# Kernel tuning notes

Measured on AMD Instinct MI355X. Metric: run time of the kernel, lower is better.

Reference implementation:

```python
import jax, jax.numpy as jnp
import numpy as np
import math

N_H = 16
REL_K = 16  # relative-position clamp window


def setup_inputs() -> dict:
    key = jax.random.key(0)
    ks = jax.random.split(key, 7)
    B, S, D = 8, 1024, 1024
    d_k = D // N_H
    scale = 0.02
    return {
        "x": jax.random.normal(ks[0], (B, S, D), dtype=jnp.float32),
        "W_attn": jax.random.normal(ks[1], (D, 3 * D), dtype=jnp.float32) * scale,
        "b_attn": jax.random.normal(ks[2], (3 * D,), dtype=jnp.float32) * scale,
        "W_proj": jax.random.normal(ks[3], (D, D), dtype=jnp.float32) * scale,
        "b_proj": jax.random.normal(ks[4], (D,), dtype=jnp.float32) * scale,
        "lut_k": jax.random.normal(ks[5], (2 * REL_K + 1, d_k), dtype=jnp.float32) * scale,
        "lut_v": jax.random.normal(ks[6], (2 * REL_K + 1, d_k), dtype=jnp.float32) * scale,
    }


def reference(x, W_attn, b_attn, W_proj, b_proj, lut_k, lut_v):
    B, S, D = x.shape
    d_k = D // N_H

    qkv = x @ W_attn + b_attn  # [B, S, 3D]
    q, k, v = jnp.split(qkv, 3, axis=-1)
    # [B, H, S, d_k]
    q = q.reshape(B, S, N_H, d_k).transpose(0, 2, 1, 3)
    k = k.reshape(B, S, N_H, d_k).transpose(0, 2, 1, 3)
    v = v.reshape(B, S, N_H, d_k).transpose(0, 2, 1, 3)

    i = jnp.arange(S)[:, None]
    j = jnp.arange(S)[None, :]
    rel = jnp.clip(j - i, -REL_K, REL_K) + REL_K  # [S, S] in [0, 2k]
    aij_k = lut_k[rel]  # [S, S, d_k]
    aij_v = lut_v[rel]  # [S, S, d_k]

    scores = jnp.einsum('bhid,bhjd->bhij', q, k)
    scores = scores + jnp.einsum('bhid,ijd->bhij', q, aij_k)
    scores = scores * (1.0 / math.sqrt(d_k))

    causal = j <= i  # [S, S]
    scores = jnp.where(causal[None, None, :, :], scores, -jnp.inf)
    attn = jax.nn.softmax(scores, axis=-1)  # [B, H, S, S]

    out = jnp.einsum('bhij,bhjd->bhid', attn, v)
    out = out + jnp.einsum('bhij,ijd->bhid', attn, aij_v)
    out = out.transpose(0, 2, 1, 3).reshape(B, S, D)
    return out @ W_proj + b_proj
```

## Files before the change

kernel.cpp:

```cpp
#include <hip/hip_runtime.h>
#include <hip/hip_bf16.h>
#include <math.h>

#define NH 16
#define S_LEN 1024
#define DK 64
#define D_MODEL 1024
#define HSZ 8388608

typedef __attribute__((ext_vector_type(8))) short bf16x8;
typedef __attribute__((ext_vector_type(4))) float f32x4;
typedef unsigned short USH;

#define EXPSCALE 0.1803368801111204f

__device__ __forceinline__ float fast_exp2(float x) {
    return __builtin_amdgcn_exp2f(x);
}

__device__ __forceinline__ short f2b(float x) {
    union { __hip_bfloat16 h; short s; } u;
    u.h = __float2bfloat16(x);
    return u.s;
}
__device__ __forceinline__ float b2f(USH u) {
    union { unsigned i; float f; } x;
    x.i = (unsigned)u << 16;
    return x.f;
}

__device__ __forceinline__ void gload16(const void* src, void* lds) {
    __builtin_amdgcn_global_load_lds(
        (const __attribute__((address_space(1))) void*)src,
        (__attribute__((address_space(3))) void*)lds,
        16, 0, 0);
}

__global__ __launch_bounds__(256)
void prep_kernel(const float* __restrict__ x, USH* __restrict__ xb,
                 const float* __restrict__ W_attn, USH* __restrict__ watt,
                 const float* __restrict__ W_proj, USH* __restrict__ wproj) {
    const int blk = blockIdx.x;
    const int t = threadIdx.x;
    if (blk < 4096) {
        const int i = (blk * 256 + t) * 8;
        const float4 a = *(const float4*)&x[i];
        const float4 b = *(const float4*)&x[i + 4];
        ushort4 o0, o1;
        o0.x = (USH)f2b(a.x); o0.y = (USH)f2b(a.y); o0.z = (USH)f2b(a.z); o0.w = (USH)f2b(a.w);
        o1.x = (USH)f2b(b.x); o1.y = (USH)f2b(b.y); o1.z = (USH)f2b(b.z); o1.w = (USH)f2b(b.w);
        *(ushort4*)&xb[i] = o0;
        *(ushort4*)&xb[i + 4] = o1;
        return;
    }
    __shared__ USH Ts[64][65];
    const float* in;
    USH* out;
    int R, C, r0, c0;
    if (blk < 4864) {
        const int idx = blk - 4096;
        in = W_attn; out = watt; R = 1024; C = 3072;
        c0 = (idx % 48) * 64; r0 = (idx / 48) * 64;
    } else {
        const int idx = blk - 4864;
        in = W_proj; out = wproj; R = 1024; C = 1024;
        c0 = (idx % 16) * 64; r0 = (idx / 16) * 64;
    }
    const int tr = t >> 4;
    const int tc4 = (t & 15) * 4;
    #pragma unroll
    for (int ph = 0; ph < 4; ++ph) {
        const int r = ph * 16 + tr;
        const float4 v = *(const float4*)&in[(size_t)(r0 + r) * C + c0 + tc4];
        Ts[tc4 + 0][r] = (USH)f2b(v.x);
        Ts[tc4 + 1][r] = (USH)f2b(v.y);
        Ts[tc4 + 2][r] = (USH)f2b(v.z);
        Ts[tc4 + 3][r] = (USH)f2b(v.w);
    }
    __syncthreads();
    #pragma unroll
    for (int ph = 0; ph < 4; ++ph) {
        const int cc = ph * 16 + tr;
        ushort4 o;
        o.x = Ts[cc][tc4 + 0]; o.y = Ts[cc][tc4 + 1];
        o.z = Ts[cc][tc4 + 2]; o.w = Ts[cc][tc4 + 3];
        *(ushort4*)&out[(size_t)(c0 + cc) * R + r0 + tc4] = o;
    }
}

template<int QKV>
__global__ __launch_bounds__(512)
void gemm256_kernel(const USH* __restrict__ A, const USH* __restrict__ Bt,
                    const float* __restrict__ bias,
                    float* __restrict__ Cf, USH* __restrict__ Cq,
                    USH* __restrict__ Ck, USH* __restrict__ Cvt,
                    int N, int NTILN) {
    __shared__ __align__(16) USH lds[36864];
    const int t = threadIdx.x;
    const int w = t >> 6, lane = t & 63, g = lane >> 4, c = lane & 15;
    const int wm = w >> 1, wn = w & 1;
    const int nwg = NTILN * 32;
    const int bid = blockIdx.x;
    const int swz = (bid & 7) * (nwg >> 3) + (bid >> 3);
    const int bn0 = (swz % NTILN) * 128;
    const int bm0 = (swz / NTILN) * 256;

    auto stage = [&](int kt, int slot) {
        const int k0 = kt * 32;
        char* base = (char*)lds + slot * 24576;
        #pragma unroll
        for (int q = 0; q < 2; ++q) {
            const int o = t * 16 + q * 8192;
            const int row = o >> 6;
            const int sc = (((o >> 4) & 3) ^ (row & 3)) * 8;
            gload16(A + (size_t)(bm0 + row) * 1024 + k0 + sc, base + o);
        }
        const int o = t * 16;
        const int row = o >> 6;
        const int sc = (((o >> 4) & 3) ^ (row & 3)) * 8;
        gload16(Bt + (size_t)(bn0 + row) * 1024 + k0 + sc, base + 16384 + o);
    };

    unsigned aoff[4], boff[4];
    #pragma unroll
    for (int i = 0; i < 4; ++i) {
        const int row = wm * 64 + i * 16 + c;
        aoff[i] = (unsigned)(row * 64) + (((unsigned)(g ^ (row & 3))) << 4);
        const int rn = wn * 64 + i * 16 + c;
        boff[i] = 16384u + (unsigned)(rn * 64) + (((unsigned)(g ^ (rn & 3))) << 4);
    }

    f32x4 acc[4][4];
    #pragma unroll
    for (int i = 0; i < 4; ++i)
        #pragma unroll
        for (int j = 0; j < 4; ++j) acc[i][j] = (f32x4)0.f;

    stage(0, 0);
    stage(1, 1);

    int cur = 0;
    for (int kt = 0; kt < 32; ++kt) {
        if (kt < 31) asm volatile("s_waitcnt vmcnt(3)" ::: "memory");
        else         asm volatile("s_waitcnt vmcnt(0)" ::: "memory");
        __builtin_amdgcn_s_barrier();

        const int slot2 = (cur + 2 >= 3) ? cur - 1 : cur + 2;
        if (kt + 2 < 32)
            stage(kt + 2, slot2);

        const char* sb = (const char*)lds + cur * 24576;
        bf16x8 af[4], bfr[4];
        #pragma unroll
        for (int i = 0; i < 4; ++i) af[i] = *(const bf16x8*)(sb + aoff[i]);
        #pragma unroll
        for (int j = 0; j < 4; ++j) bfr[j] = *(const bf16x8*)(sb + boff[j]);

        __builtin_amdgcn_s_setprio(1);
        #pragma unroll
        for (int i = 0; i < 4; ++i)
            #pragma unroll
            for (int j = 0; j < 4; ++j)
                acc[i][j] = __builtin_amdgcn_mfma_f32_16x16x32_bf16(
                    af[i], bfr[j], acc[i][j], 0, 0, 0);
        __builtin_amdgcn_s_setprio(0);

        cur = (cur + 1 == 3) ? 0 : cur + 1;
    }

    if (QKV) {
        if (bn0 < 2048) {
            #pragma unroll
            for (int i = 0; i < 4; ++i) {
                #pragma unroll
                for (int reg = 0; reg < 4; ++reg) {
                    const int m = bm0 + wm * 64 + i * 16 + g * 4 + reg;
                    const int b = m >> 10, s = m & 1023;
                    #pragma unroll
                    for (int j = 0; j < 4; ++j) {
                        const int n = bn0 + wn * 64 + j * 16 + c;
                        const float v = acc[i][j][reg] + bias[n];
                        const int which = n >> 10;
                        const int h = (n & 1023) >> 6, d = n & 63;
                        const size_t idx = (((size_t)(b * NH + h)) * S_LEN + s) * DK + d;
                        if (which == 0) Cq[idx] = (USH)f2b(v);
                        else            Ck[idx] = (USH)f2b(v);
                    }
                }
            }
        } else {
            __syncthreads();
            #pragma unroll
            for (int i = 0; i < 4; ++i) {
                const int m_local = wm * 64 + i * 16 + g * 4;
                #pragma unroll
                for (int j = 0; j < 4; ++j) {
                    const int n_local = wn * 64 + j * 16 + c;
                    const int n = bn0 + n_local;
                    ushort4 pk;
                    pk.x = (USH)f2b(acc[i][j][0] + bias[n]);
                    pk.y = (USH)f2b(acc[i][j][1] + bias[n]);
                    pk.z = (USH)f2b(acc[i][j][2] + bias[n]);
                    pk.w = (USH)f2b(acc[i][j][3] + bias[n]);
                    unsigned byte = ((unsigned)(n_local * 512 + m_local * 2))
                                  ^ (((unsigned)n_local & 7) << 4);
                    *(ushort4*)((char*)lds + byte) = pk;
                }
            }
            __syncthreads();
            const int b = bm0 >> 10, s0 = bm0 & 1023;
            const int h0 = (bn0 & 1023) >> 6;
            #pragma unroll
            for (int e = 0; e < 8; ++e) {
                const int task = e * 512 + t;
                const int n_local = task >> 5;
                const int chunk = task & 31;
                unsigned byte = ((unsigned)(n_local * 512 + chunk * 16))
                              ^ (((unsigned)n_local & 7) << 4);
                bf16x8 v = *(const bf16x8*)((char*)lds + byte);
                const int h = h0 + (n_local >> 6);
                const int d = n_local & 63;
                *(bf16x8*)&Cvt[(((size_t)(b * NH + h)) * DK + d) * S_LEN
                               + s0 + chunk * 8] = v;
            }
        }
    } else {
        #pragma unroll
        for (int i = 0; i < 4; ++i) {
            #pragma unroll
            for (int reg = 0; reg < 4; ++reg) {
                const int m = bm0 + wm * 64 + i * 16 + g * 4 + reg;
                #pragma unroll
                for (int j = 0; j < 4; ++j) {
                    const int n = bn0 + wn * 64 + j * 16 + c;
                    Cf[(size_t)m * N + n] = acc[i][j][reg] + bias[n];
                }
            }
        }
    }
}

__global__ __launch_bounds__(512, 4)
void attn_mfma_kernel(const USH* __restrict__ qb,
                      const USH* __restrict__ kbuf,
                      const USH* __restrict__ vtg,
                      const float* __restrict__ lut_k,
                      const float* __restrict__ lut_v,
                      USH* __restrict__ ao) {
    const int bid = blockIdx.x;
    const int logical = (bid & 7) * 128 + (bid >> 3);
    const int ib = 7 - (logical & 7);
    const int bh = logical >> 3;
    const int b = bh >> 4, h = bh & 15;
    const int i0 = ib * 128;
    const int t = threadIdx.x;
    const int w = t >> 6;
    const int lane = t & 63;
    const int g = lane >> 4;
    const int c = lane & 15;

    __shared__ __align__(16) char smem[77440];
    char* pb     = smem + 49152;
    char* qsb    = smem + 49152;
    char* lutkb  = smem + 8192;
    USH* qrelb   = (USH*)(smem + 65536);
    USH* lvfb    = (USH*)(smem + 70656);
    USH* tapssb  = (USH*)(smem + 72832);
    float* lsumb = (float*)(smem + 76928);

    const USH* qp  = qb   + (size_t)bh * (S_LEN * DK);
    const USH* kp  = kbuf + (size_t)bh * (S_LEN * DK);
    const USH* vtp = vtg  + (size_t)bh * (S_LEN * DK);

    auto stage = [&](int j0, int slot) {
        const int o = t * 16;
        const int row = o >> 7;
        const int chunk = (o >> 4) & 7;
        const int sc = (chunk ^ (row & 7)) * 8;
        gload16(kp + (size_t)(j0 + row) * DK + sc, smem + slot * 8192 + o);
        gload16(vtp + (size_t)row * S_LEN + j0 + sc, smem + 24576 + slot * 8192 + o);
    };

    stage(0, 0);
    for (int f = t; f < 2048; f += 512) {
        const int row = f >> 4, c4 = (f & 15) * 4;
        unsigned byte = ((unsigned)(row * 128 + c4 * 2)) ^ (((unsigned)row & 7) << 4);
        *(ushort4*)(qsb + byte) = *(const ushort4*)&qp[(size_t)(i0 + row) * DK + c4];
    }
    for (int e = t; e < 32 * 64; e += 512) {
        const int row = e >> 6, d = e & 63;
        const USH v = (row < 17) ? (USH)f2b(lut_k[row * 64 + d]) : (USH)0;
        unsigned byte = ((unsigned)(row * 128 + d * 2)) ^ (((unsigned)row & 7) << 4);
        *(USH*)(lutkb + byte) = v;
    }
    for (int e = t; e < 17 * 64; e += 512)
        lvfb[e] = (USH)f2b(lut_v[e]);
    __syncthreads();

    bf16x8 qa[2];
    {
        const int row = w * 16 + c;
        #pragma unroll
        for (int kh = 0; kh < 2; ++kh) {
            unsigned byte = ((unsigned)(row * 128 + kh * 64 + g * 16))
                          ^ (((unsigned)row & 7) << 4);
            qa[kh] = *(const bf16x8*)(qsb + byte);
        }
    }

    {
        f32x4 qr[2];
        qr[0] = (f32x4)0.f; qr[1] = (f32x4)0.f;
        #pragma unroll
        for (int sub2 = 0; sub2 < 2; ++sub2) {
            const int tap = sub2 * 16 + c;
            #pragma unroll
            for (int kh = 0; kh < 2; ++kh) {
                unsigned byte = ((unsigned)(tap * 128 + kh * 64 + g * 16))
                              ^ (((unsigned)tap & 7) << 4);
                bf16x8 lb = *(const bf16x8*)(lutkb + byte);
                qr[sub2] = __builtin_amdgcn_mfma_f32_16x16x32_bf16(
                    qa[kh], lb, qr[sub2], 0, 0, 0);
            }
        }
        #pragma unroll
        for (int sub2 = 0; sub2 < 2; ++sub2) {
            const int tap = sub2 * 16 + c;
            if (tap < 17) {
                #pragma unroll
                for (int r = 0; r < 4; ++r)
                    qrelb[(w * 16 + g * 4 + r) * 20 + tap] = (USH)f2b(qr[sub2][r]);
            }
        }
    }
    __syncthreads();

    const int il = w * 16 + c;
    const float qrel0s = b2f(qrelb[il * 20]) * EXPSCALE;

    const int NT = 2 * ib + 2;
    if (1 < NT) stage(64, 1);

    f32x4 acc[4];
    #pragma unroll
    for (int dt = 0; dt < 4; ++dt) acc[dt] = (f32x4)0.f;
    float l_r = 0.f;

    const int wrow0 = i0 + w * 16;
    int cur = 0;
    for (int tile = 0; tile < NT; ++tile) {
        const int nxt2 = tile + 2;
        const int slot2 = (cur + 2 >= 3) ? cur - 1 : cur + 2;
        if (nxt2 < NT)
            stage(nxt2 << 6, slot2);

        if (tile * 64 > wrow0 + 15) {
            if (nxt2 < NT) asm volatile("s_waitcnt vmcnt(2)" ::: "memory");
            else           asm volatile("s_waitcnt vmcnt(0)" ::: "memory");
            __builtin_amdgcn_s_barrier();
            cur = (cur + 1 == 3) ? 0 : cur + 1;
            continue;
        }

        const char* ktb = smem + cur * 8192;
        const char* vtb = smem + 24576 + cur * 8192;

        float p[4][4];
        __builtin_amdgcn_s_setprio(1);
        f32x4 s[4];
        #pragma unroll
        for (int sub = 0; sub < 4; ++sub) {
            s[sub] = (f32x4)0.f;
            const int krow = sub * 16 + c;
            #pragma unroll
            for (int kh = 0; kh < 2; ++kh) {
                unsigned byte = ((unsigned)krow << 7) + ((unsigned)kh << 6) + ((unsigned)g << 4);
                byte ^= (unsigned)(krow & 7) << 4;
                bf16x8 kb = *(const bf16x8*)(ktb + byte);
                s[sub] = __builtin_amdgcn_mfma_f32_16x16x32_bf16(kb, qa[kh], s[sub], 0, 0, 0);
            }
        }
        __builtin_amdgcn_s_setprio(0);

        if (tile * 64 + 79 <= wrow0) {
            #pragma unroll
            for (int sub = 0; sub < 4; ++sub)
                #pragma unroll
                for (int r = 0; r < 4; ++r)
                    p[sub][r] = fast_exp2(s[sub][r] * EXPSCALE + qrel0s);
        } else {
            #pragma unroll
            for (int sub = 0; sub < 4; ++sub) {
                const int jbase = tile * 64 + sub * 16 + g * 4;
                #pragma unroll
                for (int r = 0; r < 4; ++r) {
                    const int dj = jbase + r - (i0 + il);
                    int t17 = dj + 16;
                    t17 = t17 < 0 ? 0 : (t17 > 16 ? 16 : t17);
                    float pv = fast_exp2((s[sub][r] + b2f(qrelb[il * 20 + t17])) * EXPSCALE);
                    if (dj > 0) pv = 0.f;
                    p[sub][r] = pv;
                    if (dj >= -15 && dj <= 0)
                        tapssb[il * 16 + dj + 15] = (USH)f2b(pv);
                }
            }
        }

        #pragma unroll
        for (int sub = 0; sub < 4; ++sub)
            l_r += (p[sub][0] + p[sub][1]) + (p[sub][2] + p[sub][3]);

        char* pw = pb + w * 2048;
        #pragma unroll
        for (int sub = 0; sub < 4; ++sub) {
            const unsigned u0 = ((unsigned)(USH)f2b(p[sub][1]) << 16)
                              | (unsigned)(USH)f2b(p[sub][0]);
            const unsigned u1 = ((unsigned)(USH)f2b(p[sub][3]) << 16)
                              | (unsigned)(USH)f2b(p[sub][2]);
            uint2 val; val.x = u0; val.y = u1;
            unsigned byte = ((unsigned)(c * 128 + sub * 32 + g * 8))
                          ^ (((unsigned)c & 7) << 4);
            *(uint2*)(pw + byte) = val;
        }

        bf16x8 pa[2];
        #pragma unroll
        for (int jh = 0; jh < 2; ++jh) {
            unsigned byte = ((unsigned)c << 7) + ((unsigned)jh << 6) + ((unsigned)g << 4);
            byte ^= (unsigned)(c & 7) << 4;
            pa[jh] = *(const bf16x8*)(pw + byte);
        }
        __builtin_amdgcn_s_setprio(1);
        #pragma unroll
        for (int dt = 0; dt < 4; ++dt) {
            const int d = dt * 16 + c;
            #pragma unroll
            for (int jh = 0; jh < 2; ++jh) {
                unsigned byte = ((unsigned)d << 7) + ((unsigned)jh << 6) + ((unsigned)g << 4);
                byte ^= (unsigned)(d & 7) << 4;
                bf16x8 vb = *(const bf16x8*)(vtb + byte);
                acc[dt] = __builtin_amdgcn_mfma_f32_16x16x32_bf16(pa[jh], vb, acc[dt], 0, 0, 0);
            }
        }
        __builtin_amdgcn_s_setprio(0);

        if (nxt2 < NT) asm volatile("s_waitcnt vmcnt(2)" ::: "memory");
        else           asm volatile("s_waitcnt vmcnt(0)" ::: "memory");
        __builtin_amdgcn_s_barrier();
        cur = (cur + 1 == 3) ? 0 : cur + 1;
    }

    float lsum = l_r;
    lsum += __shfl_xor(lsum, 16);
    lsum += __shfl_xor(lsum, 32);
    if (g == 0) lsumb[il] = lsum;

    const int rbase = w * 16 + g * 4;
    #pragma unroll
    for (int r = 0; r < 4; ++r) {
        const int ilr = rbase + r;
        const float lsr = lsumb[w * 16 + g * 4 + r];
        float c0 = lsr;
        float tp[16];
        #pragma unroll
        for (int tap = 0; tap < 16; ++tap) {
            const int jg = i0 + ilr + tap - 15;
            const float pv = (jg >= 0) ? b2f(tapssb[ilr * 16 + tap]) : 0.f;
            tp[tap] = pv;
            c0 -= pv;
        }
        const float invl = 1.f / lsr;
        #pragma unroll
        for (int dt = 0; dt < 4; ++dt) {
            const int d = dt * 16 + c;
            float o = acc[dt][r] + c0 * b2f(lvfb[d]);
            #pragma unroll
            for (int tap = 0; tap < 16; ++tap)
                o += tp[tap] * b2f(lvfb[(tap + 1) * 64 + d]);
            o *= invl;
            ao[((size_t)b * S_LEN + (i0 + ilr)) * D_MODEL + h * DK + d] = (USH)f2b(o);
        }
    }
}

extern "C" void kernel_launch(void* const* d_in, const int* in_sizes, int n_in,
                              void* d_out, int out_size, void* d_ws, size_t ws_size,
                              hipStream_t stream) {
    const float* x      = (const float*)d_in[0];
    const float* W_attn = (const float*)d_in[1];
    const float* b_attn = (const float*)d_in[2];
    const float* W_proj = (const float*)d_in[3];
    const float* b_proj = (const float*)d_in[4];
    const float* lut_k  = (const float*)d_in[5];
    const float* lut_v  = (const float*)d_in[6];
    float* out = (float*)d_out;

    USH* qb    = (USH*)d_ws;
    USH* kb    = qb + HSZ;
    USH* vb    = kb + HSZ;
    USH* vtg   = vb + HSZ;
    USH* aob   = vtg + HSZ;
    USH* xb    = aob + HSZ;
    USH* watt  = xb + HSZ;
    USH* wproj = watt + 3145728;

    prep_kernel<<<5120, 256, 0, stream>>>(x, xb, W_attn, watt, W_proj, wproj);

    gemm256_kernel<1><<<768, 512, 0, stream>>>(
        xb, watt, b_attn, nullptr, qb, kb, vtg, 3072, 24);

    attn_mfma_kernel<<<1024, 512, 0, stream>>>(qb, kb, vtg, lut_k, lut_v, aob);

    gemm256_kernel<0><<<256, 512, 0, stream>>>(
        aob, wproj, b_proj, out, nullptr, nullptr, nullptr, 1024, 8);
}
```

Measured before the change: 172.6 us.

## Drop LDS K/V staging in attention; read K/V directly from global per wave

Restructures the attention kernel into 256-thread blocks of four independent waves, each covering 16 query rows. Each wave reads K, V^T, Q and the LUTs straight from global memory instead of cooperatively staging K/V tiles into LDS through a triple-buffered async pipeline with barriers. This removes block-wide barriers and the idle waves caused by causal imbalance inside a block, and cuts LDS use so more blocks can be resident. In exchange, the K/V reuse across waves is lost, global and L2 traffic rise, and load latency is no longer hidden by prefetching.

```diff
diff --git a/kernel.cpp b/kernel.cpp
--- a/kernel.cpp
+++ b/kernel.cpp
@@ -240,7 +240,7 @@
     }
 }
 
-__global__ __launch_bounds__(512, 4)
+__global__ __launch_bounds__(256, 4)
 void attn_mfma_kernel(const USH* __restrict__ qb,
                       const USH* __restrict__ kbuf,
                       const USH* __restrict__ vtg,
@@ -248,65 +248,31 @@
                       const float* __restrict__ lut_v,
                       USH* __restrict__ ao) {
     const int bid = blockIdx.x;
-    const int logical = (bid & 7) * 128 + (bid >> 3);
-    const int ib = 7 - (logical & 7);
-    const int bh = logical >> 3;
+    const int logical = (bid & 7) * 256 + (bid >> 3);
+    const int bh = logical >> 4;
+    const int quarter = 15 - (logical & 15);
     const int b = bh >> 4, h = bh & 15;
-    const int i0 = ib * 128;
     const int t = threadIdx.x;
     const int w = t >> 6;
     const int lane = t & 63;
     const int g = lane >> 4;
     const int c = lane & 15;
-
-    __shared__ __align__(16) char smem[77440];
-    char* pb     = smem + 49152;
-    char* qsb    = smem + 49152;
-    char* lutkb  = smem + 8192;
-    USH* qrelb   = (USH*)(smem + 65536);
-    USH* lvfb    = (USH*)(smem + 70656);
-    USH* tapssb  = (USH*)(smem + 72832);
-    float* lsumb = (float*)(smem + 76928);
+    const int wrow0 = (quarter * 4 + w) * 16;
+
+    __shared__ __align__(16) char smem[4 * 3264];
+    char* pw     = smem + w * 3264;
+    USH*  qrelw  = (USH*)(pw + 2048);
+    USH*  tapsw  = (USH*)(pw + 2688);
+    float* lsumw = (float*)(pw + 3200);
 
     const USH* qp  = qb   + (size_t)bh * (S_LEN * DK);
     const USH* kp  = kbuf + (size_t)bh * (S_LEN * DK);
     const USH* vtp = vtg  + (size_t)bh * (S_LEN * DK);
 
-    auto stage = [&](int j0, int slot) {
-        const int o = t * 16;
-        const int row = o >> 7;
-        const int chunk = (o >> 4) & 7;
-        const int sc = (chunk ^ (row & 7)) * 8;
-        gload16(kp + (size_t)(j0 + row) * DK + sc, smem + slot * 8192 + o);
-        gload16(vtp + (size_t)row * S_LEN + j0 + sc, smem + 24576 + slot * 8192 + o);
-    };
-
-    stage(0, 0);
-    for (int f = t; f < 2048; f += 512) {
-        const int row = f >> 4, c4 = (f & 15) * 4;
-        unsigned byte = ((unsigned)(row * 128 + c4 * 2)) ^ (((unsigned)row & 7) << 4);
-        *(ushort4*)(qsb + byte) = *(const ushort4*)&qp[(size_t)(i0 + row) * DK + c4];
-    }
-    for (int e = t; e < 32 * 64; e += 512) {
-        const int row = e >> 6, d = e & 63;
-        const USH v = (row < 17) ? (USH)f2b(lut_k[row * 64 + d]) : (USH)0;
-        unsigned byte = ((unsigned)(row * 128 + d * 2)) ^ (((unsigned)row & 7) << 4);
-        *(USH*)(lutkb + byte) = v;
-    }
-    for (int e = t; e < 17 * 64; e += 512)
-        lvfb[e] = (USH)f2b(lut_v[e]);
-    __syncthreads();
-
     bf16x8 qa[2];
-    {
-        const int row = w * 16 + c;
-        #pragma unroll
-        for (int kh = 0; kh < 2; ++kh) {
-            unsigned byte = ((unsigned)(row * 128 + kh * 64 + g * 16))
-                          ^ (((unsigned)row & 7) << 4);
-            qa[kh] = *(const bf16x8*)(qsb + byte);
-        }
-    }
+    #pragma unroll
+    for (int kh = 0; kh < 2; ++kh)
+        qa[kh] = *(const bf16x8*)&qp[(size_t)(wrow0 + c) * DK + kh * 32 + g * 8];
 
     {
         f32x4 qr[2];
@@ -316,9 +282,16 @@
             const int tap = sub2 * 16 + c;
             #pragma unroll
             for (int kh = 0; kh < 2; ++kh) {
-                unsigned byte = ((unsigned)(tap * 128 + kh * 64 + g * 16))
-                              ^ (((unsigned)tap & 7) << 4);
-                bf16x8 lb = *(const bf16x8*)(lutkb + byte);
+                bf16x8 lb = (bf16x8)(short)0;
+                if (tap < 17) {
+                    const float* lr = &lut_k[tap * 64 + kh * 32 + g * 8];
+                    const f32x4 lo = *(const f32x4*)lr;
+                    const f32x4 hi = *(const f32x4*)(lr + 4);
+                    lb[0] = f2b(lo[0]); lb[1] = f2b(lo[1]);
+                    lb[2] = f2b(lo[2]); lb[3] = f2b(lo[3]);
+                    lb[4] = f2b(hi[0]); lb[5] = f2b(hi[1]);
+                    lb[6] = f2b(hi[2]); lb[7] = f2b(hi[3]);
+                }
                 qr[sub2] = __builtin_amdgcn_mfma_f32_16x16x32_bf16(
                     qa[kh], lb, qr[sub2], 0, 0, 0);
             }
@@ -329,79 +302,56 @@
             if (tap < 17) {
                 #pragma unroll
                 for (int r = 0; r < 4; ++r)
-                    qrelb[(w * 16 + g * 4 + r) * 20 + tap] = (USH)f2b(qr[sub2][r]);
-            }
-        }
-    }
-    __syncthreads();
-
-    const int il = w * 16 + c;
-    const float qrel0s = b2f(qrelb[il * 20]) * EXPSCALE;
-
-    const int NT = 2 * ib + 2;
-    if (1 < NT) stage(64, 1);
+                    qrelw[(g * 4 + r) * 20 + tap] = (USH)f2b(qr[sub2][r]);
+            }
+        }
+    }
+    const float qrel0s = b2f(qrelw[c * 20]) * EXPSCALE;
 
     f32x4 acc[4];
     #pragma unroll
     for (int dt = 0; dt < 4; ++dt) acc[dt] = (f32x4)0.f;
     float l_r = 0.f;
 
-    const int wrow0 = i0 + w * 16;
-    int cur = 0;
-    for (int tile = 0; tile < NT; ++tile) {
-        const int nxt2 = tile + 2;
-        const int slot2 = (cur + 2 >= 3) ? cur - 1 : cur + 2;
-        if (nxt2 < NT)
-            stage(nxt2 << 6, slot2);
-
-        if (tile * 64 > wrow0 + 15) {
-            if (nxt2 < NT) asm volatile("s_waitcnt vmcnt(2)" ::: "memory");
-            else           asm volatile("s_waitcnt vmcnt(0)" ::: "memory");
-            __builtin_amdgcn_s_barrier();
-            cur = (cur + 1 == 3) ? 0 : cur + 1;
-            continue;
-        }
-
-        const char* ktb = smem + cur * 8192;
-        const char* vtb = smem + 24576 + cur * 8192;
+    const int NTw = (wrow0 >> 6) + 1;
+    for (int tile = 0; tile < NTw; ++tile) {
+        const int j0 = tile << 6;
 
         float p[4][4];
-        __builtin_amdgcn_s_setprio(1);
         f32x4 s[4];
         #pragma unroll
         for (int sub = 0; sub < 4; ++sub) {
             s[sub] = (f32x4)0.f;
-            const int krow = sub * 16 + c;
             #pragma unroll
             for (int kh = 0; kh < 2; ++kh) {
-                unsigned byte = ((unsigned)krow << 7) + ((unsigned)kh << 6) + ((unsigned)g << 4);
-                byte ^= (unsigned)(krow & 7) << 4;
-                bf16x8 kb = *(const bf16x8*)(ktb + byte);
-                s[sub] = __builtin_amdgcn_mfma_f32_16x16x32_bf16(kb, qa[kh], s[sub], 0, 0, 0);
-            }
-        }
-        __builtin_amdgcn_s_setprio(0);
-
-        if (tile * 64 + 79 <= wrow0) {
+                const bf16x8 kb = *(const bf16x8*)
+                    &kp[(size_t)(j0 + sub * 16 + c) * DK + kh * 32 + g * 8];
+                s[sub] = __builtin_amdgcn_mfma_f32_16x16x32_bf16(
+                    kb, qa[kh], s[sub], 0, 0, 0);
+            }
+        }
+
+        if (j0 + 79 <= wrow0) {
             #pragma unroll
             for (int sub = 0; sub < 4; ++sub)
                 #pragma unroll
                 for (int r = 0; r < 4; ++r)
                     p[sub][r] = fast_exp2(s[sub][r] * EXPSCALE + qrel0s);
         } else {
+            const int iq = wrow0 + c;
             #pragma unroll
             for (int sub = 0; sub < 4; ++sub) {
-                const int jbase = tile * 64 + sub * 16 + g * 4;
+                const int jbase = j0 + sub * 16 + g * 4;
                 #pragma unroll
                 for (int r = 0; r < 4; ++r) {
-                    const int dj = jbase + r - (i0 + il);
+                    const int dj = jbase + r - iq;
                     int t17 = dj + 16;
                     t17 = t17 < 0 ? 0 : (t17 > 16 ? 16 : t17);
-                    float pv = fast_exp2((s[sub][r] + b2f(qrelb[il * 20 + t17])) * EXPSCALE);
+                    float pv = fast_exp2((s[sub][r] + b2f(qrelw[c * 20 + t17])) * EXPSCALE);
                     if (dj > 0) pv = 0.f;
                     p[sub][r] = pv;
                     if (dj >= -15 && dj <= 0)
-                        tapssb[il * 16 + dj + 15] = (USH)f2b(pv);
+                        tapsw[c * 16 + dj + 15] = (USH)f2b(pv);
                 }
             }
         }
@@ -410,7 +360,6 @@
         for (int sub = 0; sub < 4; ++sub)
             l_r += (p[sub][0] + p[sub][1]) + (p[sub][2] + p[sub][3]);
 
-        char* pw = pb + w * 2048;
         #pragma unroll
         for (int sub = 0; sub < 4; ++sub) {
             const unsigned u0 = ((unsigned)(USH)f2b(p[sub][1]) << 16)
@@ -426,46 +375,39 @@
         bf16x8 pa[2];
         #pragma unroll
         for (int jh = 0; jh < 2; ++jh) {
-            unsigned byte = ((unsigned)c << 7) + ((unsigned)jh << 6) + ((unsigned)g << 4);
-            byte ^= (unsigned)(c & 7) << 4;
+            unsigned byte = ((unsigned)(c * 128 + jh * 64 + g * 16))
+                          ^ (((unsigned)c & 7) << 4);
             pa[jh] = *(const bf16x8*)(pw + byte);
         }
-        __builtin_amdgcn_s_setprio(1);
         #pragma unroll
         for (int dt = 0; dt < 4; ++dt) {
             const int d = dt * 16 + c;
             #pragma unroll
             for (int jh = 0; jh < 2; ++jh) {
-                unsigned byte = ((unsigned)d << 7) + ((unsigned)jh << 6) + ((unsigned)g << 4);
-                byte ^= (unsigned)(d & 7) << 4;
-                bf16x8 vb = *(const bf16x8*)(vtb + byte);
-                acc[dt] = __builtin_amdgcn_mfma_f32_16x16x32_bf16(pa[jh], vb, acc[dt], 0, 0, 0);
-            }
-        }
-        __builtin_amdgcn_s_setprio(0);
-
-        if (nxt2 < NT) asm volatile("s_waitcnt vmcnt(2)" ::: "memory");
-        else           asm volatile("s_waitcnt vmcnt(0)" ::: "memory");
-        __builtin_amdgcn_s_barrier();
-        cur = (cur + 1 == 3) ? 0 : cur + 1;
+                const bf16x8 vb = *(const bf16x8*)
+                    &vtp[(size_t)d * S_LEN + j0 + jh * 32 + g * 8];
+                acc[dt] = __builtin_amdgcn_mfma_f32_16x16x32_bf16(
+                    pa[jh], vb, acc[dt], 0, 0, 0);
+            }
+        }
     }
 
     float lsum = l_r;
     lsum += __shfl_xor(lsum, 16);
     lsum += __shfl_xor(lsum, 32);
-    if (g == 0) lsumb[il] = lsum;
-
-    const int rbase = w * 16 + g * 4;
+    if (g == 0) lsumw[c] = lsum;
+
     #pragma unroll
     for (int r = 0; r < 4; ++r) {
-        const int ilr = rbase + r;
-        const float lsr = lsumb[w * 16 + g * 4 + r];
+        const int ilr = g * 4 + r;
+        const int iq = wrow0 + ilr;
+        const float lsr = lsumw[ilr];
         float c0 = lsr;
         float tp[16];
         #pragma unroll
         for (int tap = 0; tap < 16; ++tap) {
-            const int jg = i0 + ilr + tap - 15;
-            const float pv = (jg >= 0) ? b2f(tapssb[ilr * 16 + tap]) : 0.f;
+            const int jg = iq + tap - 15;
+            const float pv = (jg >= 0) ? b2f(tapsw[ilr * 16 + tap]) : 0.f;
             tp[tap] = pv;
             c0 -= pv;
         }
@@ -473,12 +415,12 @@
         #pragma unroll
         for (int dt = 0; dt < 4; ++dt) {
             const int d = dt * 16 + c;
-            float o = acc[dt][r] + c0 * b2f(lvfb[d]);
+            float o = acc[dt][r] + c0 * lut_v[d];
             #pragma unroll
             for (int tap = 0; tap < 16; ++tap)
-                o += tp[tap] * b2f(lvfb[(tap + 1) * 64 + d]);
+                o += tp[tap] * lut_v[(tap + 1) * 64 + d];
             o *= invl;
-            ao[((size_t)b * S_LEN + (i0 + ilr)) * D_MODEL + h * DK + d] = (USH)f2b(o);
+            ao[((size_t)b * S_LEN + iq) * D_MODEL + h * DK + d] = (USH)f2b(o);
         }
     }
 }
@@ -509,7 +451,7 @@
     gemm256_kernel<1><<<768, 512, 0, stream>>>(
         xb, watt, b_attn, nullptr, qb, kb, vtg, 3072, 24);
 
-    attn_mfma_kernel<<<1024, 512, 0, stream>>>(qb, kb, vtg, lut_k, lut_v, aob);
+    attn_mfma_kernel<<<2048, 256, 0, stream>>>(qb, kb, vtg, lut_k, lut_v, aob);
 
     gemm256_kernel<0><<<256, 512, 0, stream>>>(
         aob, wproj, b_proj, out, nullptr, nullptr, nullptr, 1024, 8);
```

Result: slower. 296.6 us (+71.9%).

## Process two 16-row query sub-tiles per wave with 256-thread attention blocks

Applied to the files above, without the earlier changes.

The attention kernel now runs 4 waves of 256 threads instead of 8 waves of 512. Each wave handles 32 query rows, split into two 16-row halves, so every K and V fragment read from LDS feeds two MFMAs instead of one. Tile staging issues two loads per thread to make up for the smaller block, and the vmcnt waits are adjusted to match. This cuts LDS traffic per MFMA and the number of waves per barrier, at the cost of more registers (doubled accumulators, scores and probabilities). It also coarsens the causal tile skip, since skipping is now decided per 32 rows.

```diff
diff --git a/kernel.cpp b/kernel.cpp
--- a/kernel.cpp
+++ b/kernel.cpp
@@ -240,7 +240,7 @@
     }
 }
 
-__global__ __launch_bounds__(512, 4)
+__global__ __launch_bounds__(256, 8)
 void attn_mfma_kernel(const USH* __restrict__ qb,
                       const USH* __restrict__ kbuf,
                       const USH* __restrict__ vtg,
@@ -273,42 +273,50 @@
     const USH* vtp = vtg  + (size_t)bh * (S_LEN * DK);
 
     auto stage = [&](int j0, int slot) {
-        const int o = t * 16;
-        const int row = o >> 7;
-        const int chunk = (o >> 4) & 7;
-        const int sc = (chunk ^ (row & 7)) * 8;
-        gload16(kp + (size_t)(j0 + row) * DK + sc, smem + slot * 8192 + o);
-        gload16(vtp + (size_t)row * S_LEN + j0 + sc, smem + 24576 + slot * 8192 + o);
+        #pragma unroll
+        for (int q = 0; q < 2; ++q) {
+            const int o = q * 4096 + t * 16;
+            const int row = o >> 7;
+            const int chunk = (o >> 4) & 7;
+            const int sc = (chunk ^ (row & 7)) * 8;
+            gload16(kp + (size_t)(j0 + row) * DK + sc, smem + slot * 8192 + o);
+            gload16(vtp + (size_t)row * S_LEN + j0 + sc,
+                    smem + 24576 + slot * 8192 + o);
+        }
     };
 
     stage(0, 0);
-    for (int f = t; f < 2048; f += 512) {
+    for (int f = t; f < 2048; f += 256) {
         const int row = f >> 4, c4 = (f & 15) * 4;
         unsigned byte = ((unsigned)(row * 128 + c4 * 2)) ^ (((unsigned)row & 7) << 4);
         *(ushort4*)(qsb + byte) = *(const ushort4*)&qp[(size_t)(i0 + row) * DK + c4];
     }
-    for (int e = t; e < 32 * 64; e += 512) {
+    for (int e = t; e < 32 * 64; e += 256) {
         const int row = e >> 6, d = e & 63;
         const USH v = (row < 17) ? (USH)f2b(lut_k[row * 64 + d]) : (USH)0;
         unsigned byte = ((unsigned)(row * 128 + d * 2)) ^ (((unsigned)row & 7) << 4);
         *(USH*)(lutkb + byte) = v;
     }
-    for (int e = t; e < 17 * 64; e += 512)
+    for (int e = t; e < 17 * 64; e += 256)
         lvfb[e] = (USH)f2b(lut_v[e]);
     __syncthreads();
 
-    bf16x8 qa[2];
-    {
-        const int row = w * 16 + c;
+    const int wrow0 = i0 + w * 32;
+
+    bf16x8 qa[2][2];
+    #pragma unroll
+    for (int qh = 0; qh < 2; ++qh) {
+        const int row = w * 32 + qh * 16 + c;
         #pragma unroll
         for (int kh = 0; kh < 2; ++kh) {
             unsigned byte = ((unsigned)(row * 128 + kh * 64 + g * 16))
                           ^ (((unsigned)row & 7) << 4);
-            qa[kh] = *(const bf16x8*)(qsb + byte);
-        }
-    }
-
-    {
+            qa[qh][kh] = *(const bf16x8*)(qsb + byte);
+        }
+    }
+
+    #pragma unroll
+    for (int qh = 0; qh < 2; ++qh) {
         f32x4 qr[2];
         qr[0] = (f32x4)0.f; qr[1] = (f32x4)0.f;
         #pragma unroll
@@ -320,7 +328,7 @@
                               ^ (((unsigned)tap & 7) << 4);
                 bf16x8 lb = *(const bf16x8*)(lutkb + byte);
                 qr[sub2] = __builtin_amdgcn_mfma_f32_16x16x32_bf16(
-                    qa[kh], lb, qr[sub2], 0, 0, 0);
+                    qa[qh][kh], lb, qr[sub2], 0, 0, 0);
             }
         }
         #pragma unroll
@@ -329,24 +337,28 @@
             if (tap < 17) {
                 #pragma unroll
                 for (int r = 0; r < 4; ++r)
-                    qrelb[(w * 16 + g * 4 + r) * 20 + tap] = (USH)f2b(qr[sub2][r]);
+                    qrelb[(w * 32 + qh * 16 + g * 4 + r) * 20 + tap]
+                        = (USH)f2b(qr[sub2][r]);
             }
         }
     }
     __syncthreads();
 
-    const int il = w * 16 + c;
-    const float qrel0s = b2f(qrelb[il * 20]) * EXPSCALE;
+    float qrel0s[2];
+    #pragma unroll
+    for (int qh = 0; qh < 2; ++qh)
+        qrel0s[qh] = b2f(qrelb[(w * 32 + qh * 16 + c) * 20]) * EXPSCALE;
 
     const int NT = 2 * ib + 2;
     if (1 < NT) stage(64, 1);
 
-    f32x4 acc[4];
-    #pragma unroll
-    for (int dt = 0; dt < 4; ++dt) acc[dt] = (f32x4)0.f;
-    float l_r = 0.f;
-
-    const int wrow0 = i0 + w * 16;
+    f32x4 acc[2][4];
+    #pragma unroll
+    for (int qh = 0; qh < 2; ++qh)
+        #pragma unroll
+        for (int dt = 0; dt < 4; ++dt) acc[qh][dt] = (f32x4)0.f;
+    float l_r[2] = {0.f, 0.f};
+
     int cur = 0;
     for (int tile = 0; tile < NT; ++tile) {
         const int nxt2 = tile + 2;
@@ -354,8 +366,8 @@
         if (nxt2 < NT)
             stage(nxt2 << 6, slot2);
 
-        if (tile * 64 > wrow0 + 15) {
-            if (nxt2 < NT) asm volatile("s_waitcnt vmcnt(2)" ::: "memory");
+        if (tile * 64 > wrow0 + 31) {
+            if (nxt2 < NT) asm volatile("s_waitcnt vmcnt(4)" ::: "memory");
             else           asm volatile("s_waitcnt vmcnt(0)" ::: "memory");
             __builtin_amdgcn_s_barrier();
             cur = (cur + 1 == 3) ? 0 : cur + 1;
@@ -365,70 +377,92 @@
         const char* ktb = smem + cur * 8192;
         const char* vtb = smem + 24576 + cur * 8192;
 
-        float p[4][4];
+        float p[2][4][4];
         __builtin_amdgcn_s_setprio(1);
-        f32x4 s[4];
+        f32x4 s[2][4];
         #pragma unroll
         for (int sub = 0; sub < 4; ++sub) {
-            s[sub] = (f32x4)0.f;
+            s[0][sub] = (f32x4)0.f;
+            s[1][sub] = (f32x4)0.f;
             const int krow = sub * 16 + c;
             #pragma unroll
             for (int kh = 0; kh < 2; ++kh) {
                 unsigned byte = ((unsigned)krow << 7) + ((unsigned)kh << 6) + ((unsigned)g << 4);
                 byte ^= (unsigned)(krow & 7) << 4;
                 bf16x8 kb = *(const bf16x8*)(ktb + byte);
-                s[sub] = __builtin_amdgcn_mfma_f32_16x16x32_bf16(kb, qa[kh], s[sub], 0, 0, 0);
+                #pragma unroll
+                for (int qh = 0; qh < 2; ++qh)
+                    s[qh][sub] = __builtin_amdgcn_mfma_f32_16x16x32_bf16(
+                        kb, qa[qh][kh], s[qh][sub], 0, 0, 0);
             }
         }
         __builtin_amdgcn_s_setprio(0);
 
         if (tile * 64 + 79 <= wrow0) {
             #pragma unroll
+            for (int qh = 0; qh < 2; ++qh)
+                #pragma unroll
+                for (int sub = 0; sub < 4; ++sub)
+                    #pragma unroll
+                    for (int r = 0; r < 4; ++r)
+                        p[qh][sub][r] = fast_exp2(s[qh][sub][r] * EXPSCALE + qrel0s[qh]);
+        } else {
+            #pragma unroll
+            for (int qh = 0; qh < 2; ++qh) {
+                const int il = w * 32 + qh * 16 + c;
+                const int iq = i0 + il;
+                #pragma unroll
+                for (int sub = 0; sub < 4; ++sub) {
+                    const int jbase = tile * 64 + sub * 16 + g * 4;
+                    #pragma unroll
+                    for (int r = 0; r < 4; ++r) {
+                        const int dj = jbase + r - iq;
+                        int t17 = dj + 16;
+                        t17 = t17 < 0 ? 0 : (t17 > 16 ? 16 : t17);
+                        float pv = fast_exp2((s[qh][sub][r] + b2f(qrelb[il * 20 + t17])) * EXPSCALE);
+                        if (dj > 0) pv = 0.f;
+                        p[qh][sub][r] = pv;
+                        if (dj >= -15 && dj <= 0)
+                            tapssb[il * 16 + dj + 15] = (USH)f2b(pv);
+                    }
+                }
+            }
+        }
+
+        #pragma unroll
+        for (int qh = 0; qh < 2; ++qh)
+            #pragma unroll
             for (int sub = 0; sub < 4; ++sub)
-                #pragma unroll
-                for (int r = 0; r < 4; ++r)
-                    p[sub][r] = fast_exp2(s[sub][r] * EXPSCALE + qrel0s);
-        } else {
+                l_r[qh] += (p[qh][sub][0] + p[qh][sub][1])
+                         + (p[qh][sub][2] + p[qh][sub][3]);
+
+        char* pw = pb + w * 4096;
+        #pragma unroll
+        for (int qh = 0; qh < 2; ++qh) {
+            const int row = qh * 16 + c;
             #pragma unroll
             for (int sub = 0; sub < 4; ++sub) {
-                const int jbase = tile * 64 + sub * 16 + g * 4;
-                #pragma unroll
-                for (int r = 0; r < 4; ++r) {
-                    const int dj = jbase + r - (i0 + il);
-                    int t17 = dj + 16;
-                    t17 = t17 < 0 ? 0 : (t17 > 16 ? 16 : t17);
-                    float pv = fast_exp2((s[sub][r] + b2f(qrelb[il * 20 + t17])) * EXPSCALE);
-                    if (dj > 0) pv = 0.f;
-                    p[sub][r] = pv;
-                    if (dj >= -15 && dj <= 0)
-                        tapssb[il * 16 + dj + 15] = (USH)f2b(pv);
-                }
-            }
-        }
-
-        #pragma unroll
-        for (int sub = 0; sub < 4; ++sub)
-            l_r += (p[sub][0] + p[sub][1]) + (p[sub][2] + p[sub][3]);
-
-        char* pw = pb + w * 2048;
-        #pragma unroll
-        for (int sub = 0; sub < 4; ++sub) {
-            const unsigned u0 = ((unsigned)(USH)f2b(p[sub][1]) << 16)
-                              | (unsigned)(USH)f2b(p[sub][0]);
-            const unsigned u1 = ((unsigned)(USH)f2b(p[sub][3]) << 16)
-                              | (unsigned)(USH)f2b(p[sub][2]);
-            uint2 val; val.x = u0; val.y = u1;
-            unsigned byte = ((unsigned)(c * 128 + sub * 32 + g * 8))
-                          ^ (((unsigned)c & 7) << 4);
-            *(uint2*)(pw + byte) = val;
-        }
-
-        bf16x8 pa[2];
-        #pragma unroll
-        for (int jh = 0; jh < 2; ++jh) {
-            unsigned byte = ((unsigned)c << 7) + ((unsigned)jh << 6) + ((unsigned)g << 4);
-            byte ^= (unsigned)(c & 7) << 4;
-            pa[jh] = *(const bf16x8*)(pw + byte);
+                const unsigned u0 = ((unsigned)(USH)f2b(p[qh][sub][1]) << 16)
+                                  | (unsigned)(USH)f2b(p[qh][sub][0]);
+                const unsigned u1 = ((unsigned)(USH)f2b(p[qh][sub][3]) << 16)
+                                  | (unsigned)(USH)f2b(p[qh][sub][2]);
+                uint2 val; val.x = u0; val.y = u1;
+                unsigned byte = ((unsigned)(row * 128 + sub * 32 + g * 8))
+                              ^ (((unsigned)row & 7) << 4);
+                *(uint2*)(pw + byte) = val;
+            }
+        }
+
+        bf16x8 pa[2][2];
+        #pragma unroll
+        for (int qh = 0; qh < 2; ++qh) {
+            const int row = qh * 16 + c;
+            #pragma unroll
+            for (int jh = 0; jh < 2; ++jh) {
+                unsigned byte = ((unsigned)(row * 128 + jh * 64 + g * 16))
+                              ^ (((unsigned)row & 7) << 4);
+                pa[qh][jh] = *(const bf16x8*)(pw + byte);
+            }
         }
         __builtin_amdgcn_s_setprio(1);
         #pragma unroll
@@ -439,46 +473,55 @@
                 unsigned byte = ((unsigned)d << 7) + ((unsigned)jh << 6) + ((unsigned)g << 4);
                 byte ^= (unsigned)(d & 7) << 4;
                 bf16x8 vb = *(const bf16x8*)(vtb + byte);
-                acc[dt] = __builtin_amdgcn_mfma_f32_16x16x32_bf16(pa[jh], vb, acc[dt], 0, 0, 0);
+                #pragma unroll
+                for (int qh = 0; qh < 2; ++qh)
+                    acc[qh][dt] = __builtin_amdgcn_mfma_f32_16x16x32_bf16(
+                        pa[qh][jh], vb, acc[qh][dt], 0, 0, 0);
             }
         }
         __builtin_amdgcn_s_setprio(0);
 
-        if (nxt2 < NT) asm volatile("s_waitcnt vmcnt(2)" ::: "memory");
+        if (nxt2 < NT) asm volatile("s_waitcnt vmcnt(4)" ::: "memory");
         else           asm volatile("s_waitcnt vmcnt(0)" ::: "memory");
         __builtin_amdgcn_s_barrier();
         cur = (cur + 1 == 3) ? 0 : cur + 1;
     }
 
-    float lsum = l_r;
-    lsum += __shfl_xor(lsum, 16);
-    lsum += __shfl_xor(lsum, 32);
-    if (g == 0) lsumb[il] = lsum;
-
-    const int rbase = w * 16 + g * 4;
-    #pragma unroll
-    for (int r = 0; r < 4; ++r) {
-        const int ilr = rbase + r;
-        const float lsr = lsumb[w * 16 + g * 4 + r];
-        float c0 = lsr;
-        float tp[16];
-        #pragma unroll
-        for (int tap = 0; tap < 16; ++tap) {
-            const int jg = i0 + ilr + tap - 15;
-            const float pv = (jg >= 0) ? b2f(tapssb[ilr * 16 + tap]) : 0.f;
-            tp[tap] = pv;
-            c0 -= pv;
-        }
-        const float invl = 1.f / lsr;
-        #pragma unroll
-        for (int dt = 0; dt < 4; ++dt) {
-            const int d = dt * 16 + c;
-            float o = acc[dt][r] + c0 * b2f(lvfb[d]);
-            #pragma unroll
-            for (int tap = 0; tap < 16; ++tap)
-                o += tp[tap] * b2f(lvfb[(tap + 1) * 64 + d]);
-            o *= invl;
-            ao[((size_t)b * S_LEN + (i0 + ilr)) * D_MODEL + h * DK + d] = (USH)f2b(o);
+    #pragma unroll
+    for (int qh = 0; qh < 2; ++qh) {
+        float lsum = l_r[qh];
+        lsum += __shfl_xor(lsum, 16);
+        lsum += __shfl_xor(lsum, 32);
+        if (g == 0) lsumb[w * 32 + qh * 16 + c] = lsum;
+    }
+
+    #pragma unroll
+    for (int qh = 0; qh < 2; ++qh) {
+        #pragma unroll
+        for (int r = 0; r < 4; ++r) {
+            const int ilr = w * 32 + qh * 16 + g * 4 + r;
+            const int iq = i0 + ilr;
+            const float lsr = lsumb[ilr];
+            float c0 = lsr;
+            float tp[16];
+            #pragma unroll
+            for (int tap = 0; tap < 16; ++tap) {
+                const int jg = iq + tap - 15;
+                const float pv = (jg >= 0) ? b2f(tapssb[ilr * 16 + tap]) : 0.f;
+                tp[tap] = pv;
+                c0 -= pv;
+            }
+            const float invl = 1.f / lsr;
+            #pragma unroll
+            for (int dt = 0; dt < 4; ++dt) {
+                const int d = dt * 16 + c;
+                float o = acc[qh][dt][r] + c0 * b2f(lvfb[d]);
+                #pragma unroll
+                for (int tap = 0; tap < 16; ++tap)
+                    o += tp[tap] * b2f(lvfb[(tap + 1) * 64 + d]);
+                o *= invl;
+                ao[((size_t)b * S_LEN + iq) * D_MODEL + h * DK + d] = (USH)f2b(o);
+            }
         }
     }
 }
@@ -509,7 +552,7 @@
     gemm256_kernel<1><<<768, 512, 0, stream>>>(
         xb, watt, b_attn, nullptr, qb, kb, vtg, 3072, 24);
 
-    attn_mfma_kernel<<<1024, 512, 0, stream>>>(qb, kb, vtg, lut_k, lut_v, aob);
+    attn_mfma_kernel<<<1024, 256, 0, stream>>>(qb, kb, vtg, lut_k, lut_v, aob);
 
     gemm256_kernel<0><<<256, 512, 0, stream>>>(
         aob, wproj, b_proj, out, nullptr, nullptr, nullptr, 1024, 8);
```

Result: slower. 194.0 us (+12.4%).
